# Performance work log

Hardware: AMD Instinct MI355X
Metric: run time of the kernel (lower is better)

## Reference

```python
import jax, jax.numpy as jnp
import numpy as np

NUM_GROUPS = 131072
GROUP_SIZE = 3          # trigenic interaction queries (Dango)
HIDDEN = 128
NUM_HEADS = 4
HEAD_DIM = HIDDEN // NUM_HEADS
NUM_LAYERS = 2


def setup_inputs() -> dict:
    key = jax.random.key(0)
    ks = jax.random.split(key, 16)
    N = NUM_GROUPS * GROUP_SIZE
    H, L = HIDDEN, NUM_LAYERS
    s = 1.0 / np.sqrt(H)
    inp = {
        "gene_embeddings": jax.random.normal(ks[0], (N, H), dtype=jnp.float32),
        "batch": jnp.repeat(jnp.arange(NUM_GROUPS, dtype=jnp.int64), GROUP_SIZE),
        # static embedding Linear
        "Ws": jax.random.uniform(ks[1], (H, H), jnp.float32, -s, s),
        "bs": jnp.zeros((H,), jnp.float32),
        # per-layer attention projections, stacked over layers
        "Wq": jax.random.uniform(ks[2], (L, H, H), jnp.float32, -s, s),
        "bq": jnp.zeros((L, H), jnp.float32),
        "Wk": jax.random.uniform(ks[3], (L, H, H), jnp.float32, -s, s),
        "bk": jnp.zeros((L, H), jnp.float32),
        "Wv": jax.random.uniform(ks[4], (L, H, H), jnp.float32, -s, s),
        "bv": jnp.zeros((L, H), jnp.float32),
        "Wo": jax.random.uniform(ks[5], (L, H, H), jnp.float32, -s, s),
        "bo": jnp.zeros((L, H), jnp.float32),
        # ReZero params, init 0.01 as in module
        "beta": jnp.full((L,), 0.01, jnp.float32),
        # prediction layer (xavier_uniform)
        "Wp": jax.random.uniform(ks[6], (H, 1), jnp.float32, -np.sqrt(6.0 / (H + 1)), np.sqrt(6.0 / (H + 1))),
        "bp": jnp.zeros((1,), jnp.float32),
    }
    return inp


def _attention_layer(xg, Wq, bq, Wk, bk, Wv, bv, Wo, bo, beta):
    # xg: [G, S, H] block-diagonal groups; exclude-self masked MHA + ReZero.
    G, S, H = xg.shape
    q = (xg @ Wq + bq).reshape(G, S, NUM_HEADS, HEAD_DIM)
    k = (xg @ Wk + bk).reshape(G, S, NUM_HEADS, HEAD_DIM)
    v = (xg @ Wv + bv).reshape(G, S, NUM_HEADS, HEAD_DIM)
    scores = jnp.einsum("gqhd,gkhd->ghqk", q, k) / np.sqrt(HEAD_DIM)
    self_mask = jnp.eye(S, dtype=bool)  # exclude self-attention
    scores = jnp.where(self_mask, -jnp.inf, scores)
    attn = jax.nn.softmax(scores, axis=-1)
    attn = jnp.nan_to_num(attn, nan=0.0)  # torch.nan_to_num parity
    out = jnp.einsum("ghqk,gkhd->gqhd", attn, v).reshape(G, S, H)
    out = out @ Wo + bo
    return xg + beta * out  # ReZero residual (dropout: eval mode identity)


def reference(gene_embeddings, batch, Ws, bs, Wq, bq, Wk, bk, Wv, bv, Wo, bo, beta, Wp, bp):
    N, H = gene_embeddings.shape
    G = N // GROUP_SIZE
    static = jax.nn.relu(gene_embeddings @ Ws + bs)  # static embedding MLP
    dyn = gene_embeddings.reshape(G, GROUP_SIZE, H)
    for i in range(NUM_LAYERS):
        dyn = _attention_layer(dyn, Wq[i], bq[i], Wk[i], bk[i],
                               Wv[i], bv[i], Wo[i], bo[i], beta[i])
    dyn = dyn.reshape(N, H)
    diff_sq = (dyn - static) ** 2
    gene_scores = (diff_sq @ Wp + bp).squeeze(-1)  # [N]
    # scatter_mean over batch ids
    sums = jax.ops.segment_sum(gene_scores, batch, num_segments=G)
    cnts = jax.ops.segment_sum(jnp.ones_like(gene_scores), batch, num_segments=G)
    interaction_scores = sums / jnp.maximum(cnts, 1.0)
    return interaction_scores[:, None]  # [G, 1]
```

## Files before the change

### kernel.cpp

```cpp
#include <hip/hip_runtime.h>

#define NGROUPS 131072
#define H 128
#define SG 3
#define NHEADS 4
#define HD 32
#define GB 16
#define MR 48
#define NT 256
#define XP 132
#define BP 136
#define NLAYERS 2

typedef unsigned short u16;
typedef __bf16 bf16x8 __attribute__((ext_vector_type(8)));
typedef float floatx4 __attribute__((ext_vector_type(4)));

__device__ __forceinline__ float bf2f(u16 u) {
  union { unsigned int i; float f; } c; c.i = ((unsigned int)u) << 16; return c.f;
}
__device__ __forceinline__ u16 f2bf(float f) {
  union { float f; unsigned int i; } c; c.f = f;
  unsigned int x = c.i;
  x += 0x7fffu + ((x >> 16) & 1u);
  return (u16)(x >> 16);
}

__global__ void wconv_kernel(const float* __restrict__ Ws, const float* __restrict__ Wq,
                             const float* __restrict__ Wk, const float* __restrict__ Wv,
                             const float* __restrict__ Wo, u16* __restrict__ wt) {
  int idx = blockIdx.x * 256 + threadIdx.x;
  int slot = idx >> 14;
  int rem = idx & 16383;
  int n = rem >> 7, k = rem & 127;
  const float* src;
  if (slot == 0) src = Ws;
  else {
    int l = (slot - 1) >> 2, t = (slot - 1) & 3;
    const float* base = (t == 0) ? Wq : (t == 1) ? Wk : (t == 2) ? Wv : Wo;
    src = base + l * (H * H);
  }
  wt[idx] = f2bf(src[k * H + n]);
}

template <int MODE>
__device__ __forceinline__ void gemm_stage(
    const u16* __restrict__ A,
    const u16* __restrict__ Bw,
    const float* __restrict__ bias,
    u16* __restrict__ dst,
    float* __restrict__ xdyn,
    u16* __restrict__ xbf,
    float beta)
{
  const int lane = threadIdx.x & 63;
  const int wave = threadIdx.x >> 6;
  const int m0 = lane & 15;
  const int q8 = (lane >> 4) << 3;

  bf16x8 af[3][4];
#pragma unroll
  for (int rt = 0; rt < 3; rt++)
#pragma unroll
    for (int kk = 0; kk < 4; kk++)
      af[rt][kk] = *reinterpret_cast<const bf16x8*>(A + (rt * 16 + m0) * BP + kk * 32 + q8);

  const int col0 = wave * 16 + m0;
  const int col1 = col0 + 64;
  bf16x8 bfr[2][4];
#pragma unroll
  for (int kk = 0; kk < 4; kk++) {
    bfr[0][kk] = *reinterpret_cast<const bf16x8*>(Bw + col0 * H + kk * 32 + q8);
    bfr[1][kk] = *reinterpret_cast<const bf16x8*>(Bw + col1 * H + kk * 32 + q8);
  }

  floatx4 acc[2][3];
#pragma unroll
  for (int c = 0; c < 2; c++)
#pragma unroll
    for (int rt = 0; rt < 3; rt++)
      acc[c][rt] = (floatx4){0.f, 0.f, 0.f, 0.f};

#pragma unroll
  for (int kk = 0; kk < 4; kk++)
#pragma unroll
    for (int c = 0; c < 2; c++)
#pragma unroll
      for (int rt = 0; rt < 3; rt++)
        acc[c][rt] = __builtin_amdgcn_mfma_f32_16x16x32_bf16(af[rt][kk], bfr[c][kk], acc[c][rt], 0, 0, 0);

  const int rbase = (lane >> 4) << 2;
#pragma unroll
  for (int c = 0; c < 2; c++) {
    const int col = (c == 0) ? col0 : col1;
    const float b = bias[col];
#pragma unroll
    for (int rt = 0; rt < 3; rt++) {
#pragma unroll
      for (int r = 0; r < 4; r++) {
        const int row = rt * 16 + rbase + r;
        float v = acc[c][rt][r] + b;
        if (MODE == 0) v = fmaxf(v, 0.f);
        if (MODE <= 1) {
          dst[row * BP + col] = f2bf(v);
        } else {
          float nv = xdyn[row * XP + col] + beta * v;
          xdyn[row * XP + col] = nv;
          xbf[row * BP + col] = f2bf(nv);
        }
      }
    }
  }
}

__global__ void __launch_bounds__(NT, 2)
dango_kernel(const float* __restrict__ x, const u16* __restrict__ wt,
             const float* __restrict__ bs, const float* __restrict__ bq,
             const float* __restrict__ bk, const float* __restrict__ bv,
             const float* __restrict__ bo, const float* __restrict__ beta,
             const float* __restrict__ Wp, const float* __restrict__ bp,
             float* __restrict__ out)
{
  __shared__ float xdyn[MR][XP];
  __shared__ u16 xbf[MR][BP];
  __shared__ u16 qbuf[MR][BP];
  __shared__ u16 kbuf[MR][BP];
  __shared__ u16 stat[MR][BP];
  __shared__ float attnw[GB][NHEADS][SG][2];
  __shared__ float rowsc[MR];

  const int tid = threadIdx.x;
  const int row0 = blockIdx.x * MR;

  for (int ch = tid; ch < MR * 32; ch += NT) {
    int r = ch >> 5, c0 = (ch & 31) << 2;
    float4 v = *reinterpret_cast<const float4*>(x + (size_t)(row0 + r) * H + c0);
    *reinterpret_cast<float4*>(&xdyn[r][c0]) = v;
    ushort4 u;
    u.x = f2bf(v.x); u.y = f2bf(v.y); u.z = f2bf(v.z); u.w = f2bf(v.w);
    *reinterpret_cast<ushort4*>(&xbf[r][c0]) = u;
  }
  __syncthreads();

  gemm_stage<0>(&xbf[0][0], wt, bs, &stat[0][0], nullptr, nullptr, 0.f);

  for (int l = 0; l < NLAYERS; l++) {
    const u16* wq = wt + (size_t)(1 + l * 4 + 0) * H * H;
    const u16* wk = wt + (size_t)(1 + l * 4 + 1) * H * H;
    const u16* wv = wt + (size_t)(1 + l * 4 + 2) * H * H;
    const u16* wo = wt + (size_t)(1 + l * 4 + 3) * H * H;
    const float betal = beta[l];

    gemm_stage<1>(&xbf[0][0], wq, bq + l * H, &qbuf[0][0], nullptr, nullptr, 0.f);
    gemm_stage<1>(&xbf[0][0], wk, bk + l * H, &kbuf[0][0], nullptr, nullptr, 0.f);
    __syncthreads();

    if (tid < GB * NHEADS * SG) {
      int g = tid / (NHEADS * SG);
      int rem = tid % (NHEADS * SG);
      int h = rem / SG;
      int i = rem % SG;
      int j0 = (i == 0) ? 1 : 0;
      int j1 = (i == 2) ? 1 : 2;
      const u16* qp = &qbuf[g * 3 + i][h * HD];
      const u16* k0p = &kbuf[g * 3 + j0][h * HD];
      const u16* k1p = &kbuf[g * 3 + j1][h * HD];
      float s0 = 0.f, s1 = 0.f;
#pragma unroll
      for (int d = 0; d < HD; d++) {
        float qv = bf2f(qp[d]);
        s0 += qv * bf2f(k0p[d]);
        s1 += qv * bf2f(k1p[d]);
      }
      s0 *= 0.17677669529663687f;
      s1 *= 0.17677669529663687f;
      float mx = fmaxf(s0, s1);
      float e0 = __expf(s0 - mx), e1 = __expf(s1 - mx);
      float inv = 1.f / (e0 + e1);
      attnw[g][h][i][0] = e0 * inv;
      attnw[g][h][i][1] = e1 * inv;
    }
    __syncthreads();

    gemm_stage<1>(&xbf[0][0], wv, bv + l * H, &qbuf[0][0], nullptr, nullptr, 0.f);
    __syncthreads();

    for (int ch = tid; ch < MR * 16; ch += NT) {
      int r = ch >> 4, c0 = (ch & 15) << 3;
      int g = r / 3, i = r - g * 3, h = c0 >> 5;
      int j0 = (i == 0) ? 1 : 0;
      int j1 = (i == 2) ? 1 : 2;
      float a0 = attnw[g][h][i][0], a1 = attnw[g][h][i][1];
      const u16* v0 = &qbuf[g * 3 + j0][c0];
      const u16* v1 = &qbuf[g * 3 + j1][c0];
#pragma unroll
      for (int d = 0; d < 8; d++)
        kbuf[r][c0 + d] = f2bf(a0 * bf2f(v0[d]) + a1 * bf2f(v1[d]));
    }
    __syncthreads();

    gemm_stage<2>(&kbuf[0][0], wo, bo + l * H, nullptr, &xdyn[0][0], &xbf[0][0], betal);
    __syncthreads();
  }

  const float bpv = bp[0];
  for (int ch = tid; ch < MR * 16; ch += NT) {
    int r = ch >> 4, c0 = (ch & 15) << 3;
    float part = 0.f;
#pragma unroll
    for (int d = 0; d < 8; d++) {
      float diff = xdyn[r][c0 + d] - bf2f(stat[r][c0 + d]);
      part += diff * diff * Wp[c0 + d];
    }
    part += __shfl_xor(part, 1, 64);
    part += __shfl_xor(part, 2, 64);
    part += __shfl_xor(part, 4, 64);
    part += __shfl_xor(part, 8, 64);
    if ((tid & 15) == 0) rowsc[r] = part;
  }
  __syncthreads();
  if (tid < GB) {
    float s = (rowsc[tid * 3] + rowsc[tid * 3 + 1] + rowsc[tid * 3 + 2]) * (1.f / 3.f) + bpv;
    out[blockIdx.x * GB + tid] = s;
  }
}

extern "C" void kernel_launch(void* const* d_in, const int* in_sizes, int n_in,
                              void* d_out, int out_size, void* d_ws, size_t ws_size,
                              hipStream_t stream) {
  const float* x    = (const float*)d_in[0];
  const float* Ws   = (const float*)d_in[2];
  const float* bs   = (const float*)d_in[3];
  const float* Wq   = (const float*)d_in[4];
  const float* bq   = (const float*)d_in[5];
  const float* Wk   = (const float*)d_in[6];
  const float* bk   = (const float*)d_in[7];
  const float* Wv   = (const float*)d_in[8];
  const float* bv   = (const float*)d_in[9];
  const float* Wo   = (const float*)d_in[10];
  const float* bo   = (const float*)d_in[11];
  const float* beta = (const float*)d_in[12];
  const float* Wp   = (const float*)d_in[13];
  const float* bp   = (const float*)d_in[14];
  float* out = (float*)d_out;
  u16* wt = (u16*)d_ws;

  wconv_kernel<<<576, 256, 0, stream>>>(Ws, Wq, Wk, Wv, Wo, wt);
  dango_kernel<<<NGROUPS / GB, NT, 0, stream>>>(x, wt, bs, bq, bk, bv, bo, beta, Wp, bp, out);
}
```

Before: 639.5 us.

## Use 8 waves per block with register-resident residual stream and static output

```diff
diff --git a/kernel.cpp b/kernel.cpp
--- a/kernel.cpp
+++ b/kernel.cpp
@@ -7,8 +7,7 @@
 #define HD 32
 #define GB 16
 #define MR 48
-#define NT 256
-#define XP 132
+#define NT 512
 #define BP 136
 #define NLAYERS 2
 
@@ -43,77 +42,41 @@
   wt[idx] = f2bf(src[k * H + n]);
 }
 
-template <int MODE>
-__device__ __forceinline__ void gemm_stage(
-    const u16* __restrict__ A,
-    const u16* __restrict__ Bw,
-    const float* __restrict__ bias,
-    u16* __restrict__ dst,
-    float* __restrict__ xdyn,
-    u16* __restrict__ xbf,
-    float beta)
-{
-  const int lane = threadIdx.x & 63;
-  const int wave = threadIdx.x >> 6;
-  const int m0 = lane & 15;
-  const int q8 = (lane >> 4) << 3;
-
-  bf16x8 af[3][4];
+__device__ __forceinline__ void load_af(const u16* __restrict__ buf, int m0, int q8,
+                                        bf16x8 af[3][4]) {
 #pragma unroll
   for (int rt = 0; rt < 3; rt++)
 #pragma unroll
     for (int kk = 0; kk < 4; kk++)
-      af[rt][kk] = *reinterpret_cast<const bf16x8*>(A + (rt * 16 + m0) * BP + kk * 32 + q8);
-
-  const int col0 = wave * 16 + m0;
-  const int col1 = col0 + 64;
-  bf16x8 bfr[2][4];
-#pragma unroll
-  for (int kk = 0; kk < 4; kk++) {
-    bfr[0][kk] = *reinterpret_cast<const bf16x8*>(Bw + col0 * H + kk * 32 + q8);
-    bfr[1][kk] = *reinterpret_cast<const bf16x8*>(Bw + col1 * H + kk * 32 + q8);
-  }
-
-  floatx4 acc[2][3];
-#pragma unroll
-  for (int c = 0; c < 2; c++)
-#pragma unroll
-    for (int rt = 0; rt < 3; rt++)
-      acc[c][rt] = (floatx4){0.f, 0.f, 0.f, 0.f};
-
+      af[rt][kk] = *reinterpret_cast<const bf16x8*>(buf + (rt * 16 + m0) * BP + kk * 32 + q8);
+}
+
+__device__ __forceinline__ void mm_sub(const bf16x8 af[3][4], const u16* __restrict__ W,
+                                       int col, int q8, floatx4 acc[3]) {
+  bf16x8 b[4];
 #pragma unroll
   for (int kk = 0; kk < 4; kk++)
-#pragma unroll
-    for (int c = 0; c < 2; c++)
-#pragma unroll
-      for (int rt = 0; rt < 3; rt++)
-        acc[c][rt] = __builtin_amdgcn_mfma_f32_16x16x32_bf16(af[rt][kk], bfr[c][kk], acc[c][rt], 0, 0, 0);
-
-  const int rbase = (lane >> 4) << 2;
-#pragma unroll
-  for (int c = 0; c < 2; c++) {
-    const int col = (c == 0) ? col0 : col1;
-    const float b = bias[col];
-#pragma unroll
-    for (int rt = 0; rt < 3; rt++) {
-#pragma unroll
-      for (int r = 0; r < 4; r++) {
-        const int row = rt * 16 + rbase + r;
-        float v = acc[c][rt][r] + b;
-        if (MODE == 0) v = fmaxf(v, 0.f);
-        if (MODE <= 1) {
-          dst[row * BP + col] = f2bf(v);
-        } else {
-          float nv = xdyn[row * XP + col] + beta * v;
-          xdyn[row * XP + col] = nv;
-          xbf[row * BP + col] = f2bf(nv);
-        }
-      }
-    }
-  }
-}
-
-__global__ void __launch_bounds__(NT, 2)
+    b[kk] = *reinterpret_cast<const bf16x8*>(W + col * H + kk * 32 + q8);
+#pragma unroll
+  for (int rt = 0; rt < 3; rt++)
+    acc[rt] = (floatx4){0.f, 0.f, 0.f, 0.f};
+#pragma unroll
+  for (int kk = 0; kk < 4; kk++)
+#pragma unroll
+    for (int rt = 0; rt < 3; rt++)
+      acc[rt] = __builtin_amdgcn_mfma_f32_16x16x32_bf16(af[rt][kk], b[kk], acc[rt], 0, 0, 0);
+}
+
+__device__ __forceinline__ void store_bf(u16* __restrict__ buf, const floatx4 acc[3],
+                                         float bias, int col, int qi) {
+#pragma unroll
+  for (int rt = 0; rt < 3; rt++)
+#pragma unroll
+    for (int r = 0; r < 4; r++)
+      buf[(rt * 16 + qi * 4 + r) * BP + col] = f2bf(acc[rt][r] + bias);
+}
+
+__global__ void __launch_bounds__(NT, 4)
 dango_kernel(const float* __restrict__ x, const u16* __restrict__ wt,
              const float* __restrict__ bs, const float* __restrict__ bq,
              const float* __restrict__ bk, const float* __restrict__ bv,
@@ -121,40 +84,58 @@
              const float* __restrict__ Wp, const float* __restrict__ bp,
              float* __restrict__ out)
 {
-  __shared__ float xdyn[MR][XP];
   __shared__ u16 xbf[MR][BP];
   __shared__ u16 qbuf[MR][BP];
   __shared__ u16 kbuf[MR][BP];
-  __shared__ u16 stat[MR][BP];
   __shared__ float attnw[GB][NHEADS][SG][2];
-  __shared__ float rowsc[MR];
+  __shared__ float rowsc[MR][9];
 
   const int tid = threadIdx.x;
+  const int lane = tid & 63;
+  const int wave = tid >> 6;
+  const int m0 = lane & 15;
+  const int qi = lane >> 4;
+  const int q8 = qi << 3;
+  const int col = wave * 16 + m0;
   const int row0 = blockIdx.x * MR;
 
-  for (int ch = tid; ch < MR * 32; ch += NT) {
-    int r = ch >> 5, c0 = (ch & 31) << 2;
-    float4 v = *reinterpret_cast<const float4*>(x + (size_t)(row0 + r) * H + c0);
-    *reinterpret_cast<float4*>(&xdyn[r][c0]) = v;
-    ushort4 u;
-    u.x = f2bf(v.x); u.y = f2bf(v.y); u.z = f2bf(v.z); u.w = f2bf(v.w);
-    *reinterpret_cast<ushort4*>(&xbf[r][c0]) = u;
-  }
-  __syncthreads();
-
-  gemm_stage<0>(&xbf[0][0], wt, bs, &stat[0][0], nullptr, nullptr, 0.f);
+  float xdyn[3][4];
+#pragma unroll
+  for (int rt = 0; rt < 3; rt++)
+#pragma unroll
+    for (int r = 0; r < 4; r++) {
+      int row = rt * 16 + qi * 4 + r;
+      float v = x[(size_t)(row0 + row) * H + col];
+      xdyn[rt][r] = v;
+      xbf[row][col] = f2bf(v);
+    }
+  __syncthreads();
+
+  float stat[3][4];
+  bf16x8 af[3][4];
+  floatx4 acc[3];
+
+  load_af(&xbf[0][0], m0, q8, af);
+  __syncthreads();
+
+  mm_sub(af, wt, col, q8, acc);
+  {
+    float b = bs[col];
+#pragma unroll
+    for (int rt = 0; rt < 3; rt++)
+#pragma unroll
+      for (int r = 0; r < 4; r++)
+        stat[rt][r] = fmaxf(acc[rt][r] + b, 0.f);
+  }
+  mm_sub(af, wt + (size_t)1 * H * H, col, q8, acc);
+  store_bf(&qbuf[0][0], acc, bq[col], col, qi);
+  mm_sub(af, wt + (size_t)2 * H * H, col, q8, acc);
+  store_bf(&kbuf[0][0], acc, bk[col], col, qi);
+  mm_sub(af, wt + (size_t)3 * H * H, col, q8, acc);
+  store_bf(&xbf[0][0], acc, bv[col], col, qi);
+  __syncthreads();
 
   for (int l = 0; l < NLAYERS; l++) {
-    const u16* wq = wt + (size_t)(1 + l * 4 + 0) * H * H;
-    const u16* wk = wt + (size_t)(1 + l * 4 + 1) * H * H;
-    const u16* wv = wt + (size_t)(1 + l * 4 + 2) * H * H;
-    const u16* wo = wt + (size_t)(1 + l * 4 + 3) * H * H;
-    const float betal = beta[l];
-
-    gemm_stage<1>(&xbf[0][0], wq, bq + l * H, &qbuf[0][0], nullptr, nullptr, 0.f);
-    gemm_stage<1>(&xbf[0][0], wk, bk + l * H, &kbuf[0][0], nullptr, nullptr, 0.f);
-    __syncthreads();
-
     if (tid < GB * NHEADS * SG) {
       int g = tid / (NHEADS * SG);
       int rem = tid % (NHEADS * SG);
@@ -182,46 +163,87 @@
     }
     __syncthreads();
 
-    gemm_stage<1>(&xbf[0][0], wv, bv + l * H, &qbuf[0][0], nullptr, nullptr, 0.f);
-    __syncthreads();
-
     for (int ch = tid; ch < MR * 16; ch += NT) {
       int r = ch >> 4, c0 = (ch & 15) << 3;
       int g = r / 3, i = r - g * 3, h = c0 >> 5;
       int j0 = (i == 0) ? 1 : 0;
       int j1 = (i == 2) ? 1 : 2;
       float a0 = attnw[g][h][i][0], a1 = attnw[g][h][i][1];
-      const u16* v0 = &qbuf[g * 3 + j0][c0];
-      const u16* v1 = &qbuf[g * 3 + j1][c0];
+      const u16* v0 = &xbf[g * 3 + j0][c0];
+      const u16* v1 = &xbf[g * 3 + j1][c0];
 #pragma unroll
       for (int d = 0; d < 8; d++)
-        kbuf[r][c0 + d] = f2bf(a0 * bf2f(v0[d]) + a1 * bf2f(v1[d]));
+        qbuf[r][c0 + d] = f2bf(a0 * bf2f(v0[d]) + a1 * bf2f(v1[d]));
     }
     __syncthreads();
 
-    gemm_stage<2>(&kbuf[0][0], wo, bo + l * H, nullptr, &xdyn[0][0], &xbf[0][0], betal);
+    const u16* wo = wt + (size_t)(1 + l * 4 + 3) * H * H;
+    const float betal = beta[l];
+    load_af(&qbuf[0][0], m0, q8, af);
+    mm_sub(af, wo, col, q8, acc);
+    {
+      float b = bo[l * H + col];
+#pragma unroll
+      for (int rt = 0; rt < 3; rt++)
+#pragma unroll
+        for (int r = 0; r < 4; r++) {
+          float nv = xdyn[rt][r] + betal * (acc[rt][r] + b);
+          xdyn[rt][r] = nv;
+          xbf[(rt * 16 + qi * 4 + r)][col] = f2bf(nv);
+        }
+    }
     __syncthreads();
-  }
-
-  const float bpv = bp[0];
-  for (int ch = tid; ch < MR * 16; ch += NT) {
-    int r = ch >> 4, c0 = (ch & 15) << 3;
-    float part = 0.f;
-#pragma unroll
-    for (int d = 0; d < 8; d++) {
-      float diff = xdyn[r][c0 + d] - bf2f(stat[r][c0 + d]);
-      part += diff * diff * Wp[c0 + d];
-    }
-    part += __shfl_xor(part, 1, 64);
-    part += __shfl_xor(part, 2, 64);
-    part += __shfl_xor(part, 4, 64);
-    part += __shfl_xor(part, 8, 64);
-    if ((tid & 15) == 0) rowsc[r] = part;
+
+    if (l + 1 < NLAYERS) {
+      const u16* wq = wt + (size_t)(1 + (l + 1) * 4 + 0) * H * H;
+      const u16* wk = wt + (size_t)(1 + (l + 1) * 4 + 1) * H * H;
+      const u16* wv = wt + (size_t)(1 + (l + 1) * 4 + 2) * H * H;
+      load_af(&xbf[0][0], m0, q8, af);
+      __syncthreads();
+      mm_sub(af, wq, col, q8, acc);
+      store_bf(&qbuf[0][0], acc, bq[(l + 1) * H + col], col, qi);
+      mm_sub(af, wk, col, q8, acc);
+      store_bf(&kbuf[0][0], acc, bk[(l + 1) * H + col], col, qi);
+      mm_sub(af, wv, col, q8, acc);
+      store_bf(&xbf[0][0], acc, bv[(l + 1) * H + col], col, qi);
+      __syncthreads();
+    }
+  }
+
+  const float wpc = Wp[col];
+  float rv[3][4];
+#pragma unroll
+  for (int rt = 0; rt < 3; rt++)
+#pragma unroll
+    for (int r = 0; r < 4; r++) {
+      float d = xdyn[rt][r] - stat[rt][r];
+      rv[rt][r] = d * d * wpc;
+    }
+#pragma unroll
+  for (int mask = 1; mask <= 8; mask <<= 1)
+#pragma unroll
+    for (int rt = 0; rt < 3; rt++)
+#pragma unroll
+      for (int r = 0; r < 4; r++)
+        rv[rt][r] += __shfl_xor(rv[rt][r], mask, 64);
+  if (m0 == 0) {
+#pragma unroll
+    for (int rt = 0; rt < 3; rt++)
+#pragma unroll
+      for (int r = 0; r < 4; r++)
+        rowsc[rt * 16 + qi * 4 + r][wave] = rv[rt][r];
   }
   __syncthreads();
   if (tid < GB) {
-    float s = (rowsc[tid * 3] + rowsc[tid * 3 + 1] + rowsc[tid * 3 + 2]) * (1.f / 3.f) + bpv;
-    out[blockIdx.x * GB + tid] = s;
+    const float bpv = bp[0];
+    float s = 0.f;
+#pragma unroll
+    for (int i = 0; i < SG; i++) {
+      int row = tid * 3 + i;
+#pragma unroll
+      for (int w = 0; w < 8; w++) s += rowsc[row][w];
+    }
+    out[blockIdx.x * GB + tid] = s * (1.f / 3.f) + bpv;
   }
 }
 
```

Result: faster. 616.8 us (-3.5%).
